# Performance work log

Measured on AMD Instinct MI355X. Metric: run time of the kernel, lower is better.

## Reference

```python
import jax, jax.numpy as jnp
import numpy as np

D_MODEL = 1024
N_HEADS = 16
D_HEAD = D_MODEL // N_HEADS  # 64
M = int(round(D_HEAD * np.log(D_HEAD)))  # 266 random features, per source
KERNEL_EPS = 1e-4


def setup_inputs() -> dict:
    key = jax.random.key(0)
    ks = jax.random.split(key, 12)
    B, L = 2, 2048
    sc = 1.0 / np.sqrt(D_MODEL)
    return {
        "query": jax.random.normal(ks[0], (B, L, D_MODEL), jnp.float32),
        "key_": jax.random.normal(ks[1], (B, L, D_MODEL), jnp.float32),
        "value": jax.random.normal(ks[2], (B, L, D_MODEL), jnp.float32),
        "Wq": jax.random.normal(ks[3], (D_MODEL, D_MODEL), jnp.float32) * sc,
        "bq": jnp.zeros((D_MODEL,), jnp.float32),
        "Wk": jax.random.normal(ks[4], (D_MODEL, D_MODEL), jnp.float32) * sc,
        "bk": jnp.zeros((D_MODEL,), jnp.float32),
        "Wv": jax.random.normal(ks[5], (D_MODEL, D_MODEL), jnp.float32) * sc,
        "bv": jnp.zeros((D_MODEL,), jnp.float32),
        "Wo": jax.random.normal(ks[6], (D_MODEL, D_MODEL), jnp.float32) * sc,
        "bo": jnp.zeros((D_MODEL,), jnp.float32),
        "random_features": jax.random.normal(ks[7], (M, D_HEAD), jnp.float32),
    }


def _split_heads(x):
    # [B,L,d_model] -> [B,H,L,D]
    B, L, _ = x.shape
    return x.reshape(B, L, N_HEADS, D_HEAD).transpose(0, 2, 1, 3)


def _favor_projected(q, k, rf):
    # q,k: [B,H,L,D]; rf: [M,D]. Faithful to get_projected_queries_and_keys (kernel_type='exp').
    q = q / (D_MODEL ** 0.25)
    k = k / (D_MODEL ** 0.25)
    pq = jnp.einsum('bhld,md->bhlm', q, rf)
    pk = jnp.einsum('bhld,md->bhlm', k, rf)
    h_q = -0.5 * jnp.sum(q * q, axis=-1, keepdims=True)  # [B,H,L,1]
    h_k = -0.5 * jnp.sum(k * k, axis=-1, keepdims=True)
    q_stab = jnp.max(h_q, axis=-1, keepdims=True)  # == h_q (last dim is 1), as in source
    k_stab = jnp.max(h_k)  # global scalar, as in source
    q_ker = jnp.exp(h_q + (pq - q_stab))
    k_ker = jnp.exp(h_k + (pk - k_stab))
    c = M ** (-0.5)
    return c * (q_ker + KERNEL_EPS), c * (k_ker + KERNEL_EPS)


def _causal_favor(qp, kp, v):
    # qp,kp: [L,B,H,M]; v: [L,B,H,D]. Prefix-sum linear attention.
    # Denominator: q_prime[i] . cumsum(k_prime)[i]
    denom = jnp.einsum('lbhm,lbhm->lbh', qp, jnp.cumsum(kp, axis=0))

    # Numerator: recurrent scan carrying S = sum_j k'_j v_j^T  ([B,H,M,D])
    def step(S, inp):
        q_t, k_t, v_t = inp
        S = S + k_t[..., :, None] * v_t[..., None, :]
        out_t = jnp.einsum('bhmd,bhm->bhd', S, q_t)
        return S, out_t

    S0 = jnp.zeros(kp.shape[1:] + (v.shape[-1],), kp.dtype)
    _, num = jax.lax.scan(step, S0, (qp, kp, v))  # num: [L,B,H,D]
    return num / denom[..., None]


def reference(query, key_, value, Wq, bq, Wk, bk, Wv, bv, Wo, bo, random_features):
    B, L, _ = query.shape
    q = _split_heads(query @ Wq + bq)   # [B,H,L,D]
    k = _split_heads(key_ @ Wk + bk)
    v = _split_heads(value @ Wv + bv)
    q_prime, k_prime = _favor_projected(q, k, random_features)  # [B,H,L,M]
    # Causal path operates sequence-first: [L,B,H,*]
    qp = q_prime.transpose(2, 0, 1, 3)
    kp = k_prime.transpose(2, 0, 1, 3)
    vt = v.transpose(2, 0, 1, 3)
    out = _causal_favor(qp, kp, vt)               # [L,B,H,D]
    ctx = out.transpose(1, 0, 2, 3).reshape(B, L, D_MODEL)
    return ctx @ Wo + bo
```

## Files before the change

### kernel.cpp

```cpp
#include <hip/hip_runtime.h>
#include <hip/hip_bf16.h>

#define BATCH 2
#define SEQ 2048
#define DMODEL 1024
#define NH 16
#define HD 64
#define NRF 266
#define NRFP 288
#define SROW 320
#define CHK 128
#define NCH 16
#define NBH 32
#define NROWS 4096

constexpr float SCAL = 0.17677669529663687f;
constexpr float SCAL2 = 0.03125f;
constexpr float LN_CNORM = -2.7917480361965505f;
constexpr float CKEPS = 6.131393094576169e-6f;

typedef short bf16x8 __attribute__((ext_vector_type(8)));
typedef float f32x4 __attribute__((ext_vector_type(4)));

__device__ __forceinline__ short f2bs(float v) {
  __hip_bfloat16 h = __float2bfloat16(v);
  return *reinterpret_cast<short*>(&h);
}
__device__ __forceinline__ float bs2f(short s) {
  __hip_bfloat16 h;
  *reinterpret_cast<short*>(&h) = s;
  return __bfloat162float(h);
}
__device__ __forceinline__ void gload_lds16(const void* g, void* l) {
  __builtin_amdgcn_global_load_lds(
      (const __attribute__((address_space(1))) void*)g,
      (__attribute__((address_space(3))) void*)l, 16, 0, 0);
}

__global__ __launch_bounds__(256) void prep_kernel(
    const float* __restrict__ q, const float* __restrict__ k,
    const float* __restrict__ v, const float* __restrict__ Wq,
    const float* __restrict__ Wk, const float* __restrict__ Wv,
    const float* __restrict__ Wo, const float* __restrict__ rf,
    short* __restrict__ out, short* __restrict__ WtBase, short* __restrict__ rfb) {
  int z = blockIdx.z;
  int tid = threadIdx.x;
  if (z < 3) {
    const float* x = (z == 0) ? q : (z == 1) ? k : v;
    short* y = out + (size_t)z * NROWS * DMODEL;
    int bid = blockIdx.y * 64 + blockIdx.x;
    int i = bid * 2048 + tid * 8;
    float4 a = *(const float4*)&x[i];
    float4 b = *(const float4*)&x[i + 4];
    bf16x8 o;
    o[0] = f2bs(a.x); o[1] = f2bs(a.y); o[2] = f2bs(a.z); o[3] = f2bs(a.w);
    o[4] = f2bs(b.x); o[5] = f2bs(b.y); o[6] = f2bs(b.z); o[7] = f2bs(b.w);
    *(bf16x8*)&y[i] = o;
    if (z == 0 && bid < 72) {
      int idx = bid * 256 + tid;
      rfb[idx] = (idx < NRF * HD) ? f2bs(rf[idx] * SCAL) : (short)0;
    }
    return;
  }
  __shared__ float t[32][33];
  int wsel = (z - 3) * 2 + (blockIdx.x >> 5);
  const float* W = (wsel == 0) ? Wq : (wsel == 1) ? Wk : (wsel == 2) ? Wv : Wo;
  short* Wt = WtBase + (size_t)wsel * DMODEL * DMODEL;
  int k0 = blockIdx.y << 5, n0 = (blockIdx.x & 31) << 5;
  int tx = tid & 31, ty = tid >> 5;
#pragma unroll
  for (int rr = 0; rr < 4; ++rr) {
    int r = ty + (rr << 3);
    t[r][tx] = W[(size_t)(k0 + r) * DMODEL + n0 + tx];
  }
  __syncthreads();
#pragma unroll
  for (int rr = 0; rr < 4; ++rr) {
    int r = ty + (rr << 3);
    Wt[(size_t)(n0 + r) * DMODEL + k0 + tx] = f2bs(t[tx][r]);
  }
}

template <bool OUTBF>
__device__ __forceinline__ void gemm_core64(const short* __restrict__ A,
                                            const short* __restrict__ Bt,
                                            const float* __restrict__ bias,
                                            void* __restrict__ C, int bm, int bn) {
  __shared__ short As[2][128 * 64];
  __shared__ short Bs[2][64 * 64];
  int tid = threadIdx.x;
  int lane = tid & 63, wid = tid >> 6;
  int wr = wid >> 1, wc = wid & 1;
  f32x4 acc[4][2];
#pragma unroll
  for (int m = 0; m < 4; ++m)
#pragma unroll
    for (int n = 0; n < 2; ++n) acc[m][n] = f32x4{0.f, 0.f, 0.f, 0.f};

  size_t abase[4], bbase[2];
#pragma unroll
  for (int i = 0; i < 4; ++i) {
    int e = tid * 8 + i * 2048;
    int row = e >> 6;
    int k = (e & 63) ^ ((row & 7) << 3);
    abase[i] = (size_t)(bm + row) * DMODEL + k;
    if (i < 2) bbase[i] = (size_t)(bn + row) * DMODEL + k;
  }
  auto stage = [&](int buf, int k0) {
#pragma unroll
    for (int i = 0; i < 4; ++i)
      gload_lds16(A + abase[i] + k0, &As[buf][wid * 512 + i * 2048]);
#pragma unroll
    for (int i = 0; i < 2; ++i)
      gload_lds16(Bt + bbase[i] + k0, &Bs[buf][wid * 512 + i * 2048]);
  };

  stage(0, 0);
#pragma unroll 2
  for (int t = 0; t < 16; ++t) {
    int cur = t & 1;
    if (t < 15) {
      stage(cur ^ 1, (t + 1) * 64);
      asm volatile("s_waitcnt vmcnt(6)" ::: "memory");
    } else {
      asm volatile("s_waitcnt vmcnt(0)" ::: "memory");
    }
    __builtin_amdgcn_s_barrier();
    asm volatile("" ::: "memory");
    const short* curA = &As[cur][0];
    const short* curB = &Bs[cur][0];
#pragma unroll
    for (int ks = 0; ks < 2; ++ks) {
      int kb = ks * 32 + ((lane >> 4) << 3);
      bf16x8 af[4], bfv[2];
#pragma unroll
      for (int mf = 0; mf < 4; ++mf) {
        int row = wr * 64 + mf * 16 + (lane & 15);
        af[mf] = *(const bf16x8*)&curA[row * 64 + (kb ^ ((row & 7) << 3))];
      }
#pragma unroll
      for (int nf = 0; nf < 2; ++nf) {
        int row = wc * 32 + nf * 16 + (lane & 15);
        bfv[nf] = *(const bf16x8*)&curB[row * 64 + (kb ^ ((row & 7) << 3))];
      }
#pragma unroll
      for (int mf = 0; mf < 4; ++mf)
#pragma unroll
        for (int nf = 0; nf < 2; ++nf)
          acc[mf][nf] = __builtin_amdgcn_mfma_f32_16x16x32_bf16(af[mf], bfv[nf],
                                                                acc[mf][nf], 0, 0, 0);
    }
    __builtin_amdgcn_s_barrier();
    asm volatile("" ::: "memory");
  }
  int rbase = bm + wr * 64 + ((lane >> 4) << 2);
  int cbase = bn + wc * 32 + (lane & 15);
#pragma unroll
  for (int nf = 0; nf < 2; ++nf) {
    int col = cbase + nf * 16;
    float bv = bias[col];
#pragma unroll
    for (int mf = 0; mf < 4; ++mf)
#pragma unroll
      for (int r = 0; r < 4; ++r) {
        int row = rbase + mf * 16 + r;
        float v = acc[mf][nf][r] + bv;
        if (OUTBF)
          ((short*)C)[(size_t)row * DMODEL + col] = f2bs(v);
        else
          ((float*)C)[(size_t)row * DMODEL + col] = v;
      }
  }
}

__global__ __launch_bounds__(256) void gemm_qkv3(
    const short* __restrict__ Abase, const short* __restrict__ WtBase,
    const float* __restrict__ bq, const float* __restrict__ bk,
    const float* __restrict__ bv, short* __restrict__ OutBase) {
  int z = blockIdx.z;
  const short* A = Abase + (size_t)z * NROWS * DMODEL;
  const short* Bt = WtBase + (size_t)z * DMODEL * DMODEL;
  const float* bias = (z == 0) ? bq : (z == 1) ? bk : bv;
  short* C = OutBase + (size_t)z * NROWS * DMODEL;
  int bid = blockIdx.x + (blockIdx.y << 4);
  int swz = ((bid & 7) << 6) + (bid >> 3);
  int bn = (swz & 15) << 6;
  int bm = (swz >> 4) << 7;
  gemm_core64<true>(A, Bt, bias, C, bm, bn);
}

__global__ __launch_bounds__(256) void gemm_out(const short* __restrict__ A,
                                                const short* __restrict__ Bt,
                                                const float* __restrict__ bias,
                                                float* __restrict__ C) {
  int bid = blockIdx.x + (blockIdx.y << 4);
  int swz = ((bid & 7) << 6) + (bid >> 3);
  int bn = (swz & 15) << 6;
  int bm = (swz >> 4) << 7;
  gemm_core64<false>(A, Bt, bias, C, bm, bn);
}

__global__ __launch_bounds__(256, 1) void featmap_mfma(
    const short* __restrict__ Qproj, const short* __restrict__ Kproj,
    const short* __restrict__ rfb, short* __restrict__ Qp, short* __restrict__ Kp) {
  __shared__ short smem[26624];
  __shared__ float hks[128];
  short* As = smem;
  short* Bs = smem + 8192;
  int isK = blockIdx.z;
  const short* X = isK ? Kproj : Qproj;
  short* O = isK ? Kp : Qp;
  int bh = blockIdx.y, b = bh >> 4, h = bh & 15;
  int l0 = blockIdx.x << 7;
  int tid = threadIdx.x, lane = tid & 63, wid = tid >> 6;
  int cl = lane & 15, rq = lane >> 4;

#pragma unroll
  for (int i = 0; i < 4; ++i) {
    int e = tid * 8 + i * 2048;
    int row = e >> 6;
    int k = (e & 63) ^ ((row & 7) << 3);
    gload_lds16(X + ((size_t)b * SEQ + l0 + row) * DMODEL + h * HD + k,
                &As[wid * 512 + i * 2048]);
  }
#pragma unroll
  for (int i = 0; i < 9; ++i) {
    int e = tid * 8 + i * 2048;
    int row = e >> 6;
    int k = (e & 63) ^ ((row & 7) << 3);
    gload_lds16(rfb + row * HD + k, &Bs[wid * 512 + i * 2048]);
  }
  __syncthreads();

  int i0 = wid * 32;
  f32x4 acc[2][18];
#pragma unroll
  for (int m = 0; m < 2; ++m)
#pragma unroll
    for (int n = 0; n < 18; ++n) acc[m][n] = f32x4{0.f, 0.f, 0.f, 0.f};
#pragma unroll
  for (int ks = 0; ks < 2; ++ks) {
    int kb = ks * 32 + (rq << 3);
    int swz = (cl & 7) << 3;
    bf16x8 af[2];
#pragma unroll
    for (int mf = 0; mf < 2; ++mf) {
      int row = i0 + mf * 16 + cl;
      af[mf] = *(const bf16x8*)&As[row * 64 + (kb ^ swz)];
    }
#pragma unroll
    for (int nf = 0; nf < 18; ++nf) {
      int brow = nf * 16 + cl;
      bf16x8 bv = *(const bf16x8*)&Bs[brow * 64 + (kb ^ swz)];
#pragma unroll
      for (int mf = 0; mf < 2; ++mf)
        acc[mf][nf] = __builtin_amdgcn_mfma_f32_16x16x32_bf16(af[mf], bv,
                                                              acc[mf][nf], 0, 0, 0);
    }
  }

  if (isK) {
    int row = tid >> 1, half = tid & 1;
    const short* rp = &As[row * 64 + half * 32];
    float ss = 0.f;
#pragma unroll
    for (int g = 0; g < 4; ++g) {
      bf16x8 v = *(const bf16x8*)(rp + g * 8);
#pragma unroll
      for (int e = 0; e < 8; ++e) {
        float x = bs2f(v[e]);
        ss += x * x;
      }
    }
    ss += __shfl_xor(ss, 1);
    if (!half) hks[row] = -0.5f * SCAL2 * ss + LN_CNORM;
  }

  short* Ps = smem;
#pragma unroll
  for (int hf = 0; hf < 2; ++hf) {
    __syncthreads();
#pragma unroll
    for (int mf = 0; mf < 2; ++mf)
#pragma unroll
      for (int r = 0; r < 4; ++r) {
        int rl = i0 + mf * 16 + (rq << 2) + r;
        float addk = isK ? hks[rl] : LN_CNORM;
#pragma unroll
        for (int nf2 = 0; nf2 < 9; ++nf2) {
          int m = hf * 144 + nf2 * 16 + cl;
          float v = acc[mf][hf * 9 + nf2][r] + addk;
          float o = (m < NRF) ? (__expf(v) + CKEPS) : 0.f;
          Ps[rl * 152 + nf2 * 16 + cl] = f2bs(o);
        }
      }
    __syncthreads();
#pragma unroll
    for (int it = 0; it < 9; ++it) {
      int idx = tid + it * 256;
      int row = idx / 18, ch = idx - row * 18;
      bf16x8 val = *(const bf16x8*)&Ps[row * 152 + ch * 8];
      *(bf16x8*)&O[((size_t)bh * SEQ + l0 + row) * NRFP + hf * 144 + ch * 8] = val;
    }
  }
}

__global__ __launch_bounds__(256) void chunksum_mfma(
    const short* __restrict__ Kp, const short* __restrict__ Vb,
    short* __restrict__ Sct, float* __restrict__ ksum) {
  constexpr int ST = 70;
  __shared__ short KT[NRFP * ST];
  __shared__ short VT[HD * ST];
  int c = blockIdx.x, bh = blockIdx.y;
  int b = bh >> 4, h = bh & 15;
  int tid = threadIdx.x, lane = tid & 63, wv = tid >> 6;
  int cl = lane & 15, rq = lane >> 4;
  int irow = tid >> 2;
  int mq = tid & 3;
  size_t rowb = (size_t)bh * SEQ + (size_t)c * CHK;

  f32x4 acc[18];
#pragma unroll
  for (int m = 0; m < 18; ++m) acc[m] = f32x4{0.f, 0.f, 0.f, 0.f};
  float k1 = 0.f, k2 = 0.f;

  for (int hf = 0; hf < 2; ++hf) {
    __syncthreads();
    const short* Krow = Kp + (rowb + hf * 64 + irow) * NRFP;
#pragma unroll
    for (int cg = 0; cg < 9; ++cg) {
      int m0 = cg * 32 + mq * 8;
      bf16x8 v = *(const bf16x8*)(Krow + m0);
#pragma unroll
      for (int e = 0; e < 8; ++e) KT[(m0 + e) * ST + irow] = v[e];
    }
    const short* Vrow =
        Vb + ((size_t)b * SEQ + (size_t)c * CHK + hf * 64 + irow) * DMODEL + h * HD;
    {
      int d0 = mq * 16;
      bf16x8 v0 = *(const bf16x8*)(Vrow + d0);
      bf16x8 v1 = *(const bf16x8*)(Vrow + d0 + 8);
#pragma unroll
      for (int e = 0; e < 8; ++e) VT[(d0 + e) * ST + irow] = v0[e];
#pragma unroll
      for (int e = 0; e < 8; ++e) VT[(d0 + 8 + e) * ST + irow] = v1[e];
    }
    __syncthreads();
#pragma unroll
    for (int ks = 0; ks < 2; ++ks) {
      int kb = ks * 32 + rq * 8;
      bf16x8 bv = *(const bf16x8*)&VT[(wv * 16 + cl) * ST + kb];
#pragma unroll
      for (int mf = 0; mf < 18; ++mf) {
        bf16x8 av = *(const bf16x8*)&KT[(mf * 16 + cl) * ST + kb];
        acc[mf] = __builtin_amdgcn_mfma_f32_16x16x32_bf16(av, bv, acc[mf], 0, 0, 0);
      }
    }
    {
      const short* r1 = &KT[tid * ST];
#pragma unroll
      for (int g = 0; g < 8; ++g) {
        bf16x8 v = *(const bf16x8*)(r1 + g * 8);
#pragma unroll
        for (int e = 0; e < 8; ++e) k1 += bs2f(v[e]);
      }
      if (tid < 10) {
        const short* r2 = &KT[(256 + tid) * ST];
#pragma unroll
        for (int g = 0; g < 8; ++g) {
          bf16x8 v = *(const bf16x8*)(r2 + g * 8);
#pragma unroll
          for (int e = 0; e < 8; ++e) k2 += bs2f(v[e]);
        }
      }
    }
  }
  size_t sbase = ((size_t)bh * NCH + c) * (size_t)(HD * SROW);
  int d = wv * 16 + cl;
#pragma unroll
  for (int mf = 0; mf < 18; ++mf) {
    short4 o4 = make_short4(f2bs(acc[mf][0]), f2bs(acc[mf][1]),
                            f2bs(acc[mf][2]), f2bs(acc[mf][3]));
    *(short4*)&Sct[sbase + (size_t)d * SROW + mf * 16 + rq * 4] = o4;
  }
  size_t kbase = ((size_t)bh * NCH + c) * (size_t)NRF;
  if (tid < NRF) ksum[kbase + tid] = k1;
  if (tid < 10) ksum[kbase + 256 + tid] = k2;
}

__global__ __launch_bounds__(256) void prefix_all(const short* __restrict__ Sct,
                                                  short* __restrict__ Spt,
                                                  const float* __restrict__ ksum,
                                                  short* __restrict__ ksb) {
  int bh = blockIdx.y;
  if (blockIdx.x == 80) {
    for (int m = threadIdx.x; m < NRFP; m += 256) {
      if (m < NRF) {
        size_t base = (size_t)bh * NCH * NRF + m;
        float a = 0.f;
#pragma unroll
        for (int c = 0; c < NCH; ++c) {
          float v = ksum[base + (size_t)c * NRF];
          ksb[((size_t)bh * NCH + c) * NRFP + m] = f2bs(a);
          a += v;
        }
      } else {
#pragma unroll
        for (int c = 0; c < NCH; ++c)
          ksb[((size_t)bh * NCH + c) * NRFP + m] = 0;
      }
    }
    return;
  }
  int e = blockIdx.x * 256 + threadIdx.x;
  int col = e % SROW;
  if (col >= NRFP) {
#pragma unroll
    for (int c = 0; c < NCH; ++c)
      Spt[((size_t)bh * NCH + c) * (size_t)(HD * SROW) + e] = 0;
    return;
  }
  float a = 0.f;
#pragma unroll
  for (int c = 0; c < NCH; ++c) {
    size_t idx = ((size_t)bh * NCH + c) * (size_t)(HD * SROW) + e;
    float v = bs2f(Sct[idx]);
    Spt[idx] = f2bs(a);
    a += v;
  }
}

__global__ __launch_bounds__(256) void attn_mfma(
    const short* __restrict__ Qp, const short* __restrict__ Kp,
    const short* __restrict__ Vb, const short* __restrict__ Spt,
    const short* __restrict__ ksb, short* __restrict__ ctxb) {
  constexpr int PST = 136;
  __shared__ short Vt[64 * PST];
  __shared__ short SP[64 * SROW];
  __shared__ short Kb2[2][128 * 32];
  int c = blockIdx.x, bh = blockIdx.y;
  int b = bh >> 4, h = bh & 15;
  int tid = threadIdx.x, lane = tid & 63, wid = tid >> 6;
  int cl = lane & 15, rq = lane >> 4;
  size_t rowb = (size_t)bh * SEQ + (size_t)c * CHK;

  {
    int jj = tid >> 3, d0 = (tid & 7) << 3;
#pragma unroll
    for (int jt = 0; jt < 4; ++jt) {
      int j = jj + jt * 32;
      bf16x8 v = *(const bf16x8*)(Vb + ((size_t)b * SEQ + (size_t)c * CHK + j) * DMODEL +
                                  h * HD + d0);
#pragma unroll
      for (int e = 0; e < 8; ++e) Vt[(d0 + e) * PST + j] = v[e];
    }
  }
  const short* sg = Spt + ((size_t)bh * NCH + c) * (size_t)(HD * SROW);
#pragma unroll
  for (int i = 0; i < 10; ++i) {
    int o = tid * 8 + i * 2048;
    int d = o / SROW;
    int m = o - d * SROW;
    int ms = m ^ ((d & 7) << 3);
    gload_lds16(sg + (size_t)d * SROW + ms, &SP[wid * 512 + i * 2048]);
  }
  const short* Kbase = Kp + rowb * NRFP;
  auto stageK = [&](int buf, int k0) {
#pragma unroll
    for (int i = 0; i < 2; ++i) {
      int chunk = tid + i * 256;
      int row = chunk >> 2, cc = chunk & 3;
      int col = k0 + ((cc ^ (row & 3)) << 3);
      gload_lds16(Kbase + (size_t)row * NRFP + col,
                  &Kb2[buf][(wid * 64 + i * 256) * 8]);
    }
  };
  stageK(0, 0);

  int i0 = wid * 32;
  const short* Arow = Qp + (rowb + i0) * NRFP;
  const short* krow = ksb + ((size_t)bh * NCH + c) * NRFP;
  f32x4 accI[2][4];
  f32x4 accD[2];
  f32x4 accP[2][8];
#pragma unroll
  for (int m = 0; m < 2; ++m) {
#pragma unroll
    for (int n = 0; n < 4; ++n) accI[m][n] = f32x4{0.f, 0.f, 0.f, 0.f};
    accD[m] = f32x4{0.f, 0.f, 0.f, 0.f};
#pragma unroll
    for (int n = 0; n < 8; ++n) accP[m][n] = f32x4{0.f, 0.f, 0.f, 0.f};
  }
  for (int k9 = 0; k9 < 9; ++k9) {
    int cur = k9 & 1;
    if (k9 < 8) {
      stageK(cur ^ 1, (k9 + 1) * 32);
      asm volatile("s_waitcnt vmcnt(2)" ::: "memory");
    } else {
      asm volatile("s_waitcnt vmcnt(0)" ::: "memory");
    }
    __builtin_amdgcn_s_barrier();
    asm volatile("" ::: "memory");
    int kb = k9 * 32 + (rq << 3);
    bf16x8 af[2];
#pragma unroll
    for (int mf = 0; mf < 2; ++mf)
      af[mf] = *(const bf16x8*)(Arow + (size_t)(mf * 16 + cl) * NRFP + kb);
    bf16x8 bvD = {0, 0, 0, 0, 0, 0, 0, 0};
    if (cl == 0) bvD = *(const bf16x8*)(krow + kb);
#pragma unroll
    for (int mf = 0; mf < 2; ++mf)
      accD[mf] = __builtin_amdgcn_mfma_f32_16x16x32_bf16(af[mf], bvD, accD[mf], 0, 0, 0);
#pragma unroll
    for (int nf = 0; nf < 4; ++nf) {
      int row = nf * 16 + cl;
      bf16x8 bv = *(const bf16x8*)&SP[row * SROW + (kb ^ ((cl & 7) << 3))];
#pragma unroll
      for (int mf = 0; mf < 2; ++mf)
        accI[mf][nf] = __builtin_amdgcn_mfma_f32_16x16x32_bf16(af[mf], bv,
                                                               accI[mf][nf], 0, 0, 0);
    }
    const short* kcur = &Kb2[cur][0];
#pragma unroll
    for (int nf = 0; nf < 8; ++nf) {
      int row = nf * 16 + cl;
      bf16x8 bv = *(const bf16x8*)&kcur[row * 32 + ((rq ^ (cl & 3)) << 3)];
#pragma unroll
      for (int mf = 0; mf < 2; ++mf)
        accP[mf][nf] = __builtin_amdgcn_mfma_f32_16x16x32_bf16(af[mf], bv,
                                                               accP[mf][nf], 0, 0, 0);
    }
    __builtin_amdgcn_s_barrier();
    asm volatile("" ::: "memory");
  }

  float dtot[2][4];
#pragma unroll
  for (int mf = 0; mf < 2; ++mf)
#pragma unroll
    for (int r = 0; r < 4; ++r) {
      int rl = mf * 16 + (rq << 2) + r;
      int row = i0 + rl;
      float dsum = 0.f;
#pragma unroll
      for (int nf = 0; nf < 8; ++nf) {
        int col = nf * 16 + cl;
        float v = (col > row) ? 0.f : accP[mf][nf][r];
        dsum += v;
        SP[wid * 32 * PST + rl * PST + col] = f2bs(v);
      }
      dsum += __shfl_xor(dsum, 1);
      dsum += __shfl_xor(dsum, 2);
      dsum += __shfl_xor(dsum, 4);
      dsum += __shfl_xor(dsum, 8);
      float dden = __shfl(accD[mf][r], lane & 48);
      dtot[mf][r] = dden + dsum;
    }
  __syncthreads();

  f32x4 pacc[2][4];
#pragma unroll
  for (int m = 0; m < 2; ++m)
#pragma unroll
    for (int n = 0; n < 4; ++n) pacc[m][n] = f32x4{0.f, 0.f, 0.f, 0.f};
#pragma unroll
  for (int kk = 0; kk < 4; ++kk) {
    int kb = kk * 32 + (rq << 3);
    bf16x8 paf[2];
#pragma unroll
    for (int mf = 0; mf < 2; ++mf)
      paf[mf] = *(const bf16x8*)&SP[wid * 32 * PST + (mf * 16 + cl) * PST + kb];
#pragma unroll
    for (int nf = 0; nf < 4; ++nf) {
      bf16x8 bv = *(const bf16x8*)&Vt[(nf * 16 + cl) * PST + kb];
#pragma unroll
      for (int mf = 0; mf < 2; ++mf)
        pacc[mf][nf] = __builtin_amdgcn_mfma_f32_16x16x32_bf16(paf[mf], bv,
                                                               pacc[mf][nf], 0, 0, 0);
    }
  }
#pragma unroll
  for (int mf = 0; mf < 2; ++mf)
#pragma unroll
    for (int r = 0; r < 4; ++r) {
      int row = i0 + mf * 16 + (rq << 2) + r;
      float inv = 1.0f / dtot[mf][r];
      size_t ob = ((size_t)b * SEQ + (size_t)c * CHK + row) * DMODEL + h * HD;
#pragma unroll
      for (int nf = 0; nf < 4; ++nf) {
        int d = nf * 16 + cl;
        float v = (accI[mf][nf][r] + pacc[mf][nf][r]) * inv;
        ctxb[ob + d] = f2bs(v);
      }
    }
}

extern "C" void kernel_launch(void* const* d_in, const int* in_sizes, int n_in,
                              void* d_out, int out_size, void* d_ws, size_t ws_size,
                              hipStream_t stream) {
  (void)in_sizes; (void)n_in; (void)out_size;
  const float* query = (const float*)d_in[0];
  const float* key_  = (const float*)d_in[1];
  const float* value = (const float*)d_in[2];
  const float* Wq = (const float*)d_in[3];
  const float* bq = (const float*)d_in[4];
  const float* Wk = (const float*)d_in[5];
  const float* bk = (const float*)d_in[6];
  const float* Wv = (const float*)d_in[7];
  const float* bv = (const float*)d_in[8];
  const float* Wo = (const float*)d_in[9];
  const float* bo = (const float*)d_in[10];
  const float* rf = (const float*)d_in[11];

  constexpr size_t SZ_INBF = (size_t)NROWS * DMODEL * 2;
  constexpr size_t SZ_QP   = (size_t)NBH * SEQ * NRFP * 2;
  constexpr size_t SZ_WT   = (size_t)DMODEL * DMODEL * 2;
  constexpr size_t SZ_SCH  = (size_t)NBH * NCH * HD * SROW * 2;
  constexpr size_t SZ_KS   = (size_t)NBH * NCH * NRF * 4;
  constexpr size_t SZ_KSB  = (size_t)NBH * NCH * NRFP * 2;
  constexpr size_t SZ_RFB  = (size_t)NRFP * HD * 2;

  constexpr size_t O_QP   = 0;
  constexpr size_t O_KP   = O_QP + SZ_QP;
  constexpr size_t O_WT   = O_KP + SZ_QP;
  constexpr size_t O_QPR  = O_WT + 4 * SZ_WT;
  constexpr size_t O_SCH  = O_QPR + 3 * SZ_INBF;
  constexpr size_t O_SPR  = O_SCH + SZ_SCH;
  constexpr size_t O_KSUM = O_SPR + SZ_SCH;
  constexpr size_t O_KSB  = O_KSUM + SZ_KS;
  constexpr size_t O_CTXB = O_KSB + SZ_KSB;
  constexpr size_t O_RFB  = O_CTXB + SZ_INBF;
  constexpr size_t O_END  = O_RFB + SZ_RFB;
  if (ws_size < O_END) return;

  char* w = (char*)d_ws;
  short* Qbf  = (short*)(w + O_QP);
  short* Qp   = (short*)(w + O_QP);
  short* Kp   = (short*)(w + O_KP);
  short* WtB  = (short*)(w + O_WT);
  short* QprB = (short*)(w + O_QPR);
  short* Kpr  = (short*)(w + O_QPR + SZ_INBF);
  short* Vpr  = (short*)(w + O_QPR + 2 * SZ_INBF);
  short* Sct  = (short*)(w + O_SCH);
  short* Spt  = (short*)(w + O_SPR);
  float* ksum = (float*)(w + O_KSUM);
  short* ksb  = (short*)(w + O_KSB);
  short* ctxb = (short*)(w + O_CTXB);
  short* rfb  = (short*)(w + O_RFB);

  prep_kernel<<<dim3(64, 32, 5), 256, 0, stream>>>(query, key_, value, Wq, Wk, Wv,
                                                   Wo, rf, Qbf, WtB, rfb);
  gemm_qkv3<<<dim3(16, 32, 3), 256, 0, stream>>>(Qbf, WtB, bq, bk, bv, QprB);
  featmap_mfma<<<dim3(SEQ / 128, NBH, 2), 256, 0, stream>>>(QprB, Kpr, rfb, Qp, Kp);
  chunksum_mfma<<<dim3(NCH, NBH), 256, 0, stream>>>(Kp, Vpr, Sct, ksum);
  prefix_all<<<dim3(81, NBH), 256, 0, stream>>>(Sct, Spt, ksum, ksb);
  attn_mfma<<<dim3(NCH, NBH), 256, 0, stream>>>(Qp, Kp, Vpr, Spt, ksb, ctxb);
  gemm_out<<<dim3(16, 32), 256, 0, stream>>>(ctxb, WtB + 3 * (size_t)DMODEL * DMODEL,
                                             bo, (float*)d_out);
}
```

Before: 158.0 us.

## Fuse random-feature map into the Q/K projection GEMM epilogue

The Q and K projection GEMM blocks now keep their 128x64 head tile in shared memory and immediately run the random-feature MFMA, the key norm and the exp feature map, writing q'/k' directly. This removes the separate featmap kernel launch and the round trip of the bf16 Q/K projections through global memory. The bf16 input copy is moved to a different workspace region so it no longer aliases the feature-map output it is read alongside. In exchange, the GEMM kernel carries many more accumulator registers and a longer epilogue on two-thirds of its blocks, which may lower occupancy.

```diff
diff --git a/kernel.cpp b/kernel.cpp
--- a/kernel.cpp
+++ b/kernel.cpp
@@ -82,16 +82,14 @@
 }
 
 template <bool OUTBF>
-__device__ __forceinline__ void gemm_core64(const short* __restrict__ A,
+__device__ __forceinline__ void gemm64_body(short* smem, const short* __restrict__ A,
                                             const short* __restrict__ Bt,
                                             const float* __restrict__ bias,
-                                            void* __restrict__ C, int bm, int bn) {
-  __shared__ short As[2][128 * 64];
-  __shared__ short Bs[2][64 * 64];
+                                            void* __restrict__ C, int bm, int bn,
+                                            f32x4 (&acc)[4][2], bool writeC) {
   int tid = threadIdx.x;
   int lane = tid & 63, wid = tid >> 6;
   int wr = wid >> 1, wc = wid & 1;
-  f32x4 acc[4][2];
 #pragma unroll
   for (int m = 0; m < 4; ++m)
 #pragma unroll
@@ -109,10 +107,10 @@
   auto stage = [&](int buf, int k0) {
 #pragma unroll
     for (int i = 0; i < 4; ++i)
-      gload_lds16(A + abase[i] + k0, &As[buf][wid * 512 + i * 2048]);
+      gload_lds16(A + abase[i] + k0, smem + buf * 8192 + wid * 512 + i * 2048);
 #pragma unroll
     for (int i = 0; i < 2; ++i)
-      gload_lds16(Bt + bbase[i] + k0, &Bs[buf][wid * 512 + i * 2048]);
+      gload_lds16(Bt + bbase[i] + k0, smem + 16384 + buf * 4096 + wid * 512 + i * 2048);
   };
 
   stage(0, 0);
@@ -127,8 +125,8 @@
     }
     __builtin_amdgcn_s_barrier();
     asm volatile("" ::: "memory");
-    const short* curA = &As[cur][0];
-    const short* curB = &Bs[cur][0];
+    const short* curA = smem + cur * 8192;
+    const short* curB = smem + 16384 + cur * 4096;
 #pragma unroll
     for (int ks = 0; ks < 2; ++ks) {
       int kb = ks * 32 + ((lane >> 4) << 3);
@@ -153,6 +151,7 @@
     __builtin_amdgcn_s_barrier();
     asm volatile("" ::: "memory");
   }
+  if (!writeC) return;
   int rbase = bm + wr * 64 + ((lane >> 4) << 2);
   int cbase = bn + wc * 32 + (lane & 15);
 #pragma unroll
@@ -173,109 +172,111 @@
   }
 }
 
-__global__ __launch_bounds__(256) void gemm_qkv3(
+__global__ __launch_bounds__(256) void gemm_qkvf(
     const short* __restrict__ Abase, const short* __restrict__ WtBase,
     const float* __restrict__ bq, const float* __restrict__ bk,
-    const float* __restrict__ bv, short* __restrict__ OutBase) {
+    const float* __restrict__ bv, const short* __restrict__ rfb,
+    short* __restrict__ Vpr, short* __restrict__ Qp, short* __restrict__ Kp) {
+  __shared__ short smem[24576];
+  __shared__ float hk2[2][128];
+  __shared__ float hks[128];
   int z = blockIdx.z;
   const short* A = Abase + (size_t)z * NROWS * DMODEL;
   const short* Bt = WtBase + (size_t)z * DMODEL * DMODEL;
-  const float* bias = (z == 0) ? bq : (z == 1) ? bk : bv;
-  short* C = OutBase + (size_t)z * NROWS * DMODEL;
   int bid = blockIdx.x + (blockIdx.y << 4);
   int swz = ((bid & 7) << 6) + (bid >> 3);
   int bn = (swz & 15) << 6;
   int bm = (swz >> 4) << 7;
-  gemm_core64<true>(A, Bt, bias, C, bm, bn);
-}
-
-__global__ __launch_bounds__(256) void gemm_out(const short* __restrict__ A,
-                                                const short* __restrict__ Bt,
-                                                const float* __restrict__ bias,
-                                                float* __restrict__ C) {
-  int bid = blockIdx.x + (blockIdx.y << 4);
-  int swz = ((bid & 7) << 6) + (bid >> 3);
-  int bn = (swz & 15) << 6;
-  int bm = (swz >> 4) << 7;
-  gemm_core64<false>(A, Bt, bias, C, bm, bn);
-}
-
-__global__ __launch_bounds__(256, 1) void featmap_mfma(
-    const short* __restrict__ Qproj, const short* __restrict__ Kproj,
-    const short* __restrict__ rfb, short* __restrict__ Qp, short* __restrict__ Kp) {
-  __shared__ short smem[26624];
-  __shared__ float hks[128];
-  short* As = smem;
-  short* Bs = smem + 8192;
-  int isK = blockIdx.z;
-  const short* X = isK ? Kproj : Qproj;
-  short* O = isK ? Kp : Qp;
-  int bh = blockIdx.y, b = bh >> 4, h = bh & 15;
-  int l0 = blockIdx.x << 7;
+  f32x4 acc[4][2];
+  if (z == 2) {
+    gemm64_body<true>(smem, A, Bt, bv, Vpr, bm, bn, acc, true);
+    return;
+  }
+  const float* bias = z ? bk : bq;
+  short* O = z ? Kp : Qp;
+  gemm64_body<true>(smem, A, Bt, bias, nullptr, bm, bn, acc, false);
+  short* At = smem;
+  short* Rf = smem + 9216;
   int tid = threadIdx.x, lane = tid & 63, wid = tid >> 6;
   int cl = lane & 15, rq = lane >> 4;
-
-#pragma unroll
-  for (int i = 0; i < 4; ++i) {
-    int e = tid * 8 + i * 2048;
-    int row = e >> 6;
-    int k = (e & 63) ^ ((row & 7) << 3);
-    gload_lds16(X + ((size_t)b * SEQ + l0 + row) * DMODEL + h * HD + k,
-                &As[wid * 512 + i * 2048]);
-  }
-#pragma unroll
-  for (int i = 0; i < 9; ++i) {
-    int e = tid * 8 + i * 2048;
-    int row = e >> 6;
-    int k = (e & 63) ^ ((row & 7) << 3);
-    gload_lds16(rfb + row * HD + k, &Bs[wid * 512 + i * 2048]);
+  int wr = wid >> 1, wc = wid & 1;
+  int wrs = wr * 64 + (rq << 2);
+#pragma unroll
+  for (int nf = 0; nf < 2; ++nf) {
+    int col = wc * 32 + nf * 16 + cl;
+    float bv = bias[bn + col];
+#pragma unroll
+    for (int mf = 0; mf < 4; ++mf)
+#pragma unroll
+      for (int r = 0; r < 4; ++r)
+        At[(wrs + mf * 16 + r) * 72 + col] = f2bs(acc[mf][nf][r] + bv);
+  }
+  if (z == 1) {
+    float b0 = bias[bn + wc * 32 + cl], b1 = bias[bn + wc * 32 + 16 + cl];
+#pragma unroll
+    for (int mf = 0; mf < 4; ++mf)
+#pragma unroll
+      for (int r = 0; r < 4; ++r) {
+        float v0 = acc[mf][0][r] + b0;
+        float v1 = acc[mf][1][r] + b1;
+        float ss = v0 * v0 + v1 * v1;
+        ss += __shfl_xor(ss, 1);
+        ss += __shfl_xor(ss, 2);
+        ss += __shfl_xor(ss, 4);
+        ss += __shfl_xor(ss, 8);
+        if (cl == 0) hk2[wc][wrs + mf * 16 + r] = ss;
+      }
   }
   __syncthreads();
-
-  int i0 = wid * 32;
-  f32x4 acc[2][18];
+  if (z == 1 && tid < 128)
+    hks[tid] = -0.5f * SCAL2 * (hk2[0][tid] + hk2[1][tid]) + LN_CNORM;
+
+  int i0f = wid * 32;
+  f32x4 fa[2][18];
 #pragma unroll
   for (int m = 0; m < 2; ++m)
 #pragma unroll
-    for (int n = 0; n < 18; ++n) acc[m][n] = f32x4{0.f, 0.f, 0.f, 0.f};
-#pragma unroll
-  for (int ks = 0; ks < 2; ++ks) {
-    int kb = ks * 32 + (rq << 3);
-    int swz = (cl & 7) << 3;
-    bf16x8 af[2];
-#pragma unroll
-    for (int mf = 0; mf < 2; ++mf) {
-      int row = i0 + mf * 16 + cl;
-      af[mf] = *(const bf16x8*)&As[row * 64 + (kb ^ swz)];
-    }
-#pragma unroll
-    for (int nf = 0; nf < 18; ++nf) {
-      int brow = nf * 16 + cl;
-      bf16x8 bv = *(const bf16x8*)&Bs[brow * 64 + (kb ^ swz)];
+    for (int n = 0; n < 18; ++n) fa[m][n] = f32x4{0.f, 0.f, 0.f, 0.f};
+#pragma unroll
+  for (int hf = 0; hf < 2; ++hf) {
+    if (hf) __syncthreads();
+#pragma unroll
+    for (int i = 0; i < 4; ++i) {
+      int ch = tid + i * 256;
+      int row = ch >> 3, c8 = ch & 7;
+      gload_lds16(rfb + (size_t)(hf * 144 + row) * HD + ((c8 ^ (row & 7)) << 3),
+                  Rf + (wid * 512 + i * 2048));
+    }
+    if (tid < 128) {
+      int ch = 1024 + tid;
+      int row = ch >> 3, c8 = ch & 7;
+      gload_lds16(rfb + (size_t)(hf * 144 + row) * HD + ((c8 ^ (row & 7)) << 3),
+                  Rf + (1024 * 8 + (tid >> 6) * 512 + ((tid & 63) << 3)));
+    }
+    asm volatile("s_waitcnt vmcnt(0)" ::: "memory");
+    __builtin_amdgcn_s_barrier();
+    asm volatile("" ::: "memory");
+#pragma unroll
+    for (int ks = 0; ks < 2; ++ks) {
+      int kb = ks * 32 + (rq << 3);
+      bf16x8 af[2];
 #pragma unroll
       for (int mf = 0; mf < 2; ++mf)
-        acc[mf][nf] = __builtin_amdgcn_mfma_f32_16x16x32_bf16(af[mf], bv,
-                                                              acc[mf][nf], 0, 0, 0);
-    }
-  }
-
-  if (isK) {
-    int row = tid >> 1, half = tid & 1;
-    const short* rp = &As[row * 64 + half * 32];
-    float ss = 0.f;
-#pragma unroll
-    for (int g = 0; g < 4; ++g) {
-      bf16x8 v = *(const bf16x8*)(rp + g * 8);
-#pragma unroll
-      for (int e = 0; e < 8; ++e) {
-        float x = bs2f(v[e]);
-        ss += x * x;
-      }
-    }
-    ss += __shfl_xor(ss, 1);
-    if (!half) hks[row] = -0.5f * SCAL2 * ss + LN_CNORM;
-  }
-
+        af[mf] = *(const bf16x8*)&At[(i0f + mf * 16 + cl) * 72 + kb];
+#pragma unroll
+      for (int nf = 0; nf < 9; ++nf) {
+        int brow = nf * 16 + cl;
+        bf16x8 bv = *(const bf16x8*)&Rf[brow * 64 + (kb ^ ((cl & 7) << 3))];
+#pragma unroll
+        for (int mf = 0; mf < 2; ++mf)
+          fa[mf][hf * 9 + nf] = __builtin_amdgcn_mfma_f32_16x16x32_bf16(
+              af[mf], bv, fa[mf][hf * 9 + nf], 0, 0, 0);
+      }
+    }
+  }
+
+  int bh = ((bm >> 11) * NH) + (bn >> 6);
+  int l0 = bm & (SEQ - 1);
   short* Ps = smem;
 #pragma unroll
   for (int hf = 0; hf < 2; ++hf) {
@@ -284,12 +285,12 @@
     for (int mf = 0; mf < 2; ++mf)
 #pragma unroll
       for (int r = 0; r < 4; ++r) {
-        int rl = i0 + mf * 16 + (rq << 2) + r;
-        float addk = isK ? hks[rl] : LN_CNORM;
+        int rl = i0f + mf * 16 + (rq << 2) + r;
+        float addk = z ? hks[rl] : LN_CNORM;
 #pragma unroll
         for (int nf2 = 0; nf2 < 9; ++nf2) {
           int m = hf * 144 + nf2 * 16 + cl;
-          float v = acc[mf][hf * 9 + nf2][r] + addk;
+          float v = fa[mf][hf * 9 + nf2][r] + addk;
           float o = (m < NRF) ? (__expf(v) + CKEPS) : 0.f;
           Ps[rl * 152 + nf2 * 16 + cl] = f2bs(o);
         }
@@ -303,6 +304,19 @@
       *(bf16x8*)&O[((size_t)bh * SEQ + l0 + row) * NRFP + hf * 144 + ch * 8] = val;
     }
   }
+}
+
+__global__ __launch_bounds__(256) void gemm_out(const short* __restrict__ A,
+                                                const short* __restrict__ Bt,
+                                                const float* __restrict__ bias,
+                                                float* __restrict__ C) {
+  __shared__ short smem[24576];
+  int bid = blockIdx.x + (blockIdx.y << 4);
+  int swz = ((bid & 7) << 6) + (bid >> 3);
+  int bn = (swz & 15) << 6;
+  int bm = (swz >> 4) << 7;
+  f32x4 acc[4][2];
+  gemm64_body<false>(smem, A, Bt, bias, C, bm, bn, acc, true);
 }
 
 __global__ __launch_bounds__(256) void chunksum_mfma(
@@ -638,8 +652,6 @@
   short* Qp   = (short*)(w + O_QP);
   short* Kp   = (short*)(w + O_KP);
   short* WtB  = (short*)(w + O_WT);
-  short* QprB = (short*)(w + O_QPR);
-  short* Kpr  = (short*)(w + O_QPR + SZ_INBF);
   short* Vpr  = (short*)(w + O_QPR + 2 * SZ_INBF);
   short* Sct  = (short*)(w + O_SCH);
   short* Spt  = (short*)(w + O_SPR);
@@ -648,10 +660,15 @@
   short* ctxb = (short*)(w + O_CTXB);
   short* rfb  = (short*)(w + O_RFB);
 
+  Qp = (short*)(w + O_QPR);
+  short* QbfX = (short*)(w + O_SCH);
+  Qbf = QbfX;
+  Qp  = (short*)(w + O_QP);
+
   prep_kernel<<<dim3(64, 32, 5), 256, 0, stream>>>(query, key_, value, Wq, Wk, Wv,
                                                    Wo, rf, Qbf, WtB, rfb);
-  gemm_qkv3<<<dim3(16, 32, 3), 256, 0, stream>>>(Qbf, WtB, bq, bk, bv, QprB);
-  featmap_mfma<<<dim3(SEQ / 128, NBH, 2), 256, 0, stream>>>(QprB, Kpr, rfb, Qp, Kp);
+  gemm_qkvf<<<dim3(16, 32, 3), 256, 0, stream>>>(Qbf, WtB, bq, bk, bv, rfb, Vpr,
+                                                 Qp, Kp);
   chunksum_mfma<<<dim3(NCH, NBH), 256, 0, stream>>>(Kp, Vpr, Sct, ksum);
   prefix_all<<<dim3(81, NBH), 256, 0, stream>>>(Sct, Spt, ksum, ksb);
   attn_mfma<<<dim3(NCH, NBH), 256, 0, stream>>>(Qp, Kp, Vpr, Spt, ksb, ctxb);
```

New measurement: 151.1 us. -4.4%, faster.
